# Kernel optimization log

Measured on AMD Instinct MI355X. Metric: run time of the kernel, lower is better.

The kernel has to match this reference:

```python
import jax, jax.numpy as jnp
import numpy as np

SCALE_FACTORS = (1, 2, 4)
N, T, F = 4096, 128, 128
MARKET = 64
MIX = sum(T // k for k in SCALE_FACTORS)  # 224


def hardswish(x):
    return x * jnp.clip(x + 3.0, 0.0, 6.0) * (1.0 / 6.0)


def layernorm2d(x, g, b, eps=1e-5):
    # LayerNorm with normalized_shape == last two dims (as in torch nn.LayerNorm((A, B)))
    mu = jnp.mean(x, axis=(-2, -1), keepdims=True)
    var = jnp.var(x, axis=(-2, -1), keepdims=True)
    return (x - mu) * jax.lax.rsqrt(var + eps) * g + b


def setup_inputs() -> dict:
    key = jax.random.key(0)
    ks = jax.random.split(key, 32)
    inp = {"x": jax.random.normal(ks[0], (N, T, F), jnp.float32)}
    i = 1
    for si, k in enumerate(SCALE_FACTORS):
        tk = T // k
        inp[f"cw{si}"] = jax.random.normal(ks[i], (F, F, k), jnp.float32) * 0.05; i += 1
        inp[f"cb{si}"] = jnp.zeros((F,), jnp.float32)
        inp[f"lg{si}"] = jnp.ones((tk, F), jnp.float32)
        inp[f"lb{si}"] = jnp.zeros((tk, F), jnp.float32)
        inp[f"L1_{si}"] = jax.random.normal(ks[i], (tk, tk), jnp.float32) * 0.01; i += 1
        inp[f"L2_{si}"] = jax.random.normal(ks[i], (tk, tk), jnp.float32) * 0.01; i += 1
    inp["fc_w"] = jax.random.normal(ks[i], (1, F), jnp.float32) * 0.05; i += 1
    inp["fc_b"] = jnp.zeros((1,), jnp.float32)
    inp["sm_lg"] = jnp.ones((N, MIX), jnp.float32)
    inp["sm_lb"] = jnp.zeros((N, MIX), jnp.float32)
    inp["M1"] = jax.random.normal(ks[i], (MARKET, N), jnp.float32); i += 1
    inp["M2"] = jax.random.normal(ks[i], (N, MARKET), jnp.float32); i += 1
    inp["sm_fc_w"] = jax.random.normal(ks[i], (1, 2 * MIX), jnp.float32) * 0.02; i += 1
    inp["sm_fc_b"] = jnp.zeros((1,), jnp.float32)
    return inp


def _forward(x, cw0, cb0, lg0, lb0, L1_0, L2_0,
             cw1, cb1, lg1, lb1, L1_1, L2_1,
             cw2, cb2, lg2, lb2, L1_2, L2_2,
             fc_w, fc_b, sm_lg, sm_lb, M1, M2, sm_fc_w, sm_fc_b):
    n, t, f = x.shape
    per_scale = ((cw0, cb0, lg0, lb0, L1_0, L2_0),
                 (cw1, cb1, lg1, lb1, L1_1, L2_1),
                 (cw2, cb2, lg2, lb2, L1_2, L2_2))
    parts = []
    for k, (cw, cb, lg, lb, L1, L2) in zip(SCALE_FACTORS, per_scale):
        tk = t // k
        # Conv1d(kernel=k, stride=k) == blockwise contraction over non-overlapping windows
        xr = x.transpose(0, 2, 1).reshape(n, f, tk, k)          # (n, F_in, tk, k)
        xt = jnp.einsum('nitk,oik->nto', xr, cw) + cb            # (n, tk, F)
        # TimeMixing: ragged prefix loop == single lower-triangular matmul over time
        mask = jnp.tril(jnp.ones((tk, tk), x.dtype))
        h = layernorm2d(xt, lg, lb)
        u = hardswish(jnp.einsum('ts,nsf->ntf', L1 * mask, h))
        v = jnp.einsum('ts,nsf->ntf', L2 * mask, u)
        xt = xt + v
        parts.append(xt @ fc_w[0] + fc_b[0])                     # (n, tk)
    h = jnp.concatenate(parts, axis=1)                           # (n, MIX)
    # StockMixing
    hn = layernorm2d(h, sm_lg, sm_lb)
    z = M2 @ hardswish(M1 @ hn)                                  # (n, MIX)
    out = jnp.concatenate([h, h + z], axis=1)                    # (n, 2*MIX)
    return out @ sm_fc_w[0][:, None] + sm_fc_b                   # (n, 1)


def reference(x, cw0, cb0, lg0, lb0, L1_0, L2_0,
              cw1, cb1, lg1, lb1, L1_1, L2_1,
              cw2, cb2, lg2, lb2, L1_2, L2_2,
              fc_w, fc_b, sm_lg, sm_lb, M1, M2, sm_fc_w, sm_fc_b):
    return _forward(x, cw0, cb0, lg0, lb0, L1_0, L2_0,
                    cw1, cb1, lg1, lb1, L1_1, L2_1,
                    cw2, cb2, lg2, lb2, L1_2, L2_2,
                    fc_w, fc_b, sm_lg, sm_lb, M1, M2, sm_fc_w, sm_fc_b)
```

## Files before the change

### kernel.cpp

```cpp
#include <hip/hip_runtime.h>
#include <stdint.h>

typedef __attribute__((ext_vector_type(8))) short short8;
typedef __attribute__((ext_vector_type(4))) float f32x4;

__device__ __forceinline__ unsigned short f2bf(float f) {
  union { float f; unsigned int i; } v; v.f = f;
  return (unsigned short)((v.i + 0x7FFFu + ((v.i >> 16) & 1u)) >> 16);
}
__device__ __forceinline__ float hswish(float x) {
  float t = fminf(fmaxf(x + 3.f, 0.f), 6.f);
  return x * t * (1.f / 6.f);
}
__device__ __forceinline__ short8 ldcvt8(const float* __restrict__ p) {
  float4 v0 = *(const float4*)p;
  float4 v1 = *(const float4*)(p + 4);
  short8 r;
  r[0] = (short)f2bf(v0.x); r[1] = (short)f2bf(v0.y);
  r[2] = (short)f2bf(v0.z); r[3] = (short)f2bf(v0.w);
  r[4] = (short)f2bf(v1.x); r[5] = (short)f2bf(v1.y);
  r[6] = (short)f2bf(v1.z); r[7] = (short)f2bf(v1.w);
  return r;
}

__global__ void prep_kernel(const float* __restrict__ cw0, const float* __restrict__ cw1,
                            const float* __restrict__ cw2,
                            const float* __restrict__ L1_0, const float* __restrict__ L2_0,
                            const float* __restrict__ L1_1, const float* __restrict__ L2_1,
                            const float* __restrict__ L1_2, const float* __restrict__ L2_2,
                            unsigned short* __restrict__ ws16) {
  int idx = blockIdx.x * 256 + threadIdx.x;
  if (idx < 16384) {
    ws16[idx] = f2bf(cw0[idx]);
  } else if (idx < 49152) {
    int t = idx - 16384; int o = t >> 8, m = t & 255, j = m >> 7, i = m & 127;
    ws16[idx] = f2bf(cw1[(o * 128 + i) * 2 + j]);
  } else if (idx < 114688) {
    int t = idx - 49152; int o = t >> 9, m = t & 511, j = m >> 7, i = m & 127;
    ws16[idx] = f2bf(cw2[(o * 128 + i) * 4 + j]);
  } else if (idx < 131072) {
    int u = idx - 114688; int t = u >> 7, s = u & 127;
    ws16[idx] = (s <= t) ? f2bf(L1_0[u]) : (unsigned short)0;
  } else if (idx < 147456) {
    int u = idx - 131072; int t = u >> 7, s = u & 127;
    ws16[idx] = (s <= t) ? f2bf(L2_0[u]) : (unsigned short)0;
  } else if (idx < 151552) {
    int u = idx - 147456; int t = u >> 6, s = u & 63;
    ws16[idx] = (s <= t) ? f2bf(L1_1[u]) : (unsigned short)0;
  } else if (idx < 155648) {
    int u = idx - 151552; int t = u >> 6, s = u & 63;
    ws16[idx] = (s <= t) ? f2bf(L2_1[u]) : (unsigned short)0;
  } else if (idx < 156672) {
    int u = idx - 155648; int t = u >> 5, s = u & 31;
    ws16[idx] = (s <= t) ? f2bf(L1_2[u]) : (unsigned short)0;
  } else if (idx < 157696) {
    int u = idx - 156672; int t = u >> 5, s = u & 31;
    ws16[idx] = (s <= t) ? f2bf(L2_2[u]) : (unsigned short)0;
  }
}

template <int S>
__device__ __forceinline__ void scale_pass(
    const float* __restrict__ xn,
    const float* __restrict__ cb, const float* __restrict__ lg, const float* __restrict__ lb,
    const unsigned short* __restrict__ cwLT,
    const unsigned short* __restrict__ L1b, const unsigned short* __restrict__ L2b,
    unsigned short* __restrict__ HT, float* __restrict__ scr, float* __restrict__ part,
    float* __restrict__ hout, float fcb,
    int wave, int lane, int quad, int l16, int tid) {
  constexpr int K  = 128 << S;
  constexpr int TK = 128 >> S;
  constexpr int nT = (S == 0) ? 4 : (S == 1) ? 2 : 1;
  constexpr int NK = K / 32;
  constexpr int NTK = TK / 32;
  constexpr int CMASK = TK / 8 - 1;

  const int Tb = (wave & 1) * nT;
  const int Ob = (wave >> 1) * 4;

  __syncthreads();
  if (tid < TK) part[tid] = 0.f;

  f32x4 acc[nT][4];
#pragma unroll
  for (int tt = 0; tt < nT; ++tt)
#pragma unroll
    for (int oo = 0; oo < 4; ++oo) acc[tt][oo] = (f32x4){0.f, 0.f, 0.f, 0.f};

#pragma unroll
  for (int ks = 0; ks < NK; ++ks) {
    short8 a[nT];
#pragma unroll
    for (int tt = 0; tt < nT; ++tt) {
      int t = (Tb + tt) * 16 + l16;
      a[tt] = ldcvt8(xn + t * K + ks * 32 + quad * 8);
    }
#pragma unroll
    for (int oo = 0; oo < 4; ++oo) {
      int o = (Ob + oo) * 16 + l16;
      short8 b = *(const short8*)&cwLT[o * K + ks * 32 + quad * 8];
#pragma unroll
      for (int tt = 0; tt < nT; ++tt)
        acc[tt][oo] = __builtin_amdgcn_mfma_f32_16x16x32_bf16(a[tt], b, acc[tt][oo], 0, 0, 0);
    }
  }

  float sum = 0.f, ss = 0.f;
#pragma unroll
  for (int oo = 0; oo < 4; ++oo) {
    float cbv = cb[(Ob + oo) * 16 + l16];
#pragma unroll
    for (int tt = 0; tt < nT; ++tt)
#pragma unroll
      for (int r = 0; r < 4; ++r) {
        float v = acc[tt][oo][r] + cbv;
        acc[tt][oo][r] = v;
        sum += v; ss += v * v;
      }
  }
#pragma unroll
  for (int m = 32; m >= 1; m >>= 1) { sum += __shfl_xor(sum, m); ss += __shfl_xor(ss, m); }
  if (lane == 0) { scr[256 + wave * 2] = sum; scr[257 + wave * 2] = ss; }
  __syncthreads();
  if (tid == 0) {
    float Sm = scr[256] + scr[258] + scr[260] + scr[262];
    float Sq = scr[257] + scr[259] + scr[261] + scr[263];
    float mu = Sm / (float)(TK * 128);
    float var = Sq / (float)(TK * 128) - mu * mu;
    scr[264] = mu; scr[265] = rsqrtf(var + 1e-5f);
  }
  __syncthreads();
  const float mu = scr[264], rsig = scr[265];

#pragma unroll
  for (int tt = 0; tt < nT; ++tt)
#pragma unroll
    for (int r = 0; r < 4; ++r) {
      float v = 0.f;
#pragma unroll
      for (int oo = 0; oo < 4; ++oo) v += acc[tt][oo][r] * scr[(Ob + oo) * 16 + l16];
      v += __shfl_xor(v, 1); v += __shfl_xor(v, 2);
      v += __shfl_xor(v, 4); v += __shfl_xor(v, 8);
      if (l16 == 0) atomicAdd(&part[(Tb + tt) * 16 + quad * 4 + r], v);
    }

#pragma unroll
  for (int tt = 0; tt < nT; ++tt)
#pragma unroll
    for (int oo = 0; oo < 4; ++oo) {
      int f = (Ob + oo) * 16 + l16;
      int kf = (f ^ (f >> 3)) & CMASK;
#pragma unroll
      for (int r = 0; r < 4; ++r) {
        int t = (Tb + tt) * 16 + quad * 4 + r;
        float hv = (acc[tt][oo][r] - mu) * rsig * lg[t * 128 + f] + lb[t * 128 + f];
        HT[f * TK + (((t >> 3) ^ kf) << 3) + (t & 7)] = f2bf(hv);
      }
    }
  __syncthreads();

#pragma unroll
  for (int tt = 0; tt < nT; ++tt)
#pragma unroll
    for (int oo = 0; oo < 4; ++oo) acc[tt][oo] = (f32x4){0.f, 0.f, 0.f, 0.f};
#pragma unroll
  for (int ks = 0; ks < NTK; ++ks) {
    int k0 = ks * 32;
    if (k0 > (Tb + nT - 1) * 16 + 15) continue;
    short8 a[nT];
#pragma unroll
    for (int tt = 0; tt < nT; ++tt)
      if (k0 <= (Tb + tt) * 16 + 15) {
        int t = (Tb + tt) * 16 + l16;
        a[tt] = *(const short8*)&L1b[t * TK + k0 + quad * 8];
      }
#pragma unroll
    for (int oo = 0; oo < 4; ++oo) {
      int f = (Ob + oo) * 16 + l16;
      int kf = (f ^ (f >> 3)) & CMASK;
      short8 b = *(const short8*)&HT[f * TK + (((ks * 4 + quad) ^ kf) << 3)];
#pragma unroll
      for (int tt = 0; tt < nT; ++tt)
        if (k0 <= (Tb + tt) * 16 + 15)
          acc[tt][oo] = __builtin_amdgcn_mfma_f32_16x16x32_bf16(a[tt], b, acc[tt][oo], 0, 0, 0);
    }
  }
  __syncthreads();

#pragma unroll
  for (int tt = 0; tt < nT; ++tt)
#pragma unroll
    for (int oo = 0; oo < 4; ++oo) {
      int f = (Ob + oo) * 16 + l16;
      int kf = (f ^ (f >> 3)) & CMASK;
#pragma unroll
      for (int r = 0; r < 4; ++r) {
        int t = (Tb + tt) * 16 + quad * 4 + r;
        HT[f * TK + (((t >> 3) ^ kf) << 3) + (t & 7)] = f2bf(hswish(acc[tt][oo][r]));
      }
    }
  __syncthreads();

#pragma unroll
  for (int tt = 0; tt < nT; ++tt)
#pragma unroll
    for (int oo = 0; oo < 4; ++oo) acc[tt][oo] = (f32x4){0.f, 0.f, 0.f, 0.f};
#pragma unroll
  for (int ks = 0; ks < NTK; ++ks) {
    int k0 = ks * 32;
    if (k0 > (Tb + nT - 1) * 16 + 15) continue;
    short8 a[nT];
#pragma unroll
    for (int tt = 0; tt < nT; ++tt)
      if (k0 <= (Tb + tt) * 16 + 15) {
        int t = (Tb + tt) * 16 + l16;
        a[tt] = *(const short8*)&L2b[t * TK + k0 + quad * 8];
      }
#pragma unroll
    for (int oo = 0; oo < 4; ++oo) {
      int f = (Ob + oo) * 16 + l16;
      int kf = (f ^ (f >> 3)) & CMASK;
      short8 b = *(const short8*)&HT[f * TK + (((ks * 4 + quad) ^ kf) << 3)];
#pragma unroll
      for (int tt = 0; tt < nT; ++tt)
        if (k0 <= (Tb + tt) * 16 + 15)
          acc[tt][oo] = __builtin_amdgcn_mfma_f32_16x16x32_bf16(a[tt], b, acc[tt][oo], 0, 0, 0);
    }
  }

#pragma unroll
  for (int tt = 0; tt < nT; ++tt)
#pragma unroll
    for (int r = 0; r < 4; ++r) {
      float v = 0.f;
#pragma unroll
      for (int oo = 0; oo < 4; ++oo) v += acc[tt][oo][r] * scr[(Ob + oo) * 16 + l16];
      v += __shfl_xor(v, 1); v += __shfl_xor(v, 2);
      v += __shfl_xor(v, 4); v += __shfl_xor(v, 8);
      if (l16 == 0) atomicAdd(&part[(Tb + tt) * 16 + quad * 4 + r], v);
    }
  __syncthreads();
  if (tid < TK) hout[tid] = part[tid] + fcb;
}

__launch_bounds__(256, 2)
__global__ void s1_fused(const float* __restrict__ x,
                         const float* __restrict__ cb0, const float* __restrict__ lg0, const float* __restrict__ lb0,
                         const float* __restrict__ cb1, const float* __restrict__ lg1, const float* __restrict__ lb1,
                         const float* __restrict__ cb2, const float* __restrict__ lg2, const float* __restrict__ lb2,
                         const float* __restrict__ fc_w, const float* __restrict__ fc_b,
                         const unsigned short* __restrict__ ws16,
                         float* __restrict__ h_out) {
  __shared__ unsigned short HT[128 * 128];
  __shared__ float scr[268];
  const int tid = threadIdx.x, wave = tid >> 6, lane = tid & 63;
  const int quad = lane >> 4, l16 = lane & 15;
  const int n = blockIdx.x;
  const float* xn = x + (size_t)n * 16384;
  if (tid < 128) scr[tid] = fc_w[tid];
  float* part = scr + 128;
  const float fcb = fc_b[0];
  float* hout = h_out + (size_t)n * 224;

  scale_pass<0>(xn, cb0, lg0, lb0, ws16, ws16 + 114688, ws16 + 131072,
                HT, scr, part, hout, fcb, wave, lane, quad, l16, tid);
  scale_pass<1>(xn, cb1, lg1, lb1, ws16 + 16384, ws16 + 147456, ws16 + 151552,
                HT, scr, part, hout + 128, fcb, wave, lane, quad, l16, tid);
  scale_pass<2>(xn, cb2, lg2, lb2, ws16 + 49152, ws16 + 155648, ws16 + 156672,
                HT, scr, part, hout + 192, fcb, wave, lane, quad, l16, tid);
}

__global__ void stats_kernel(const float* __restrict__ h, float* __restrict__ stats) {
  int base = blockIdx.x * 4096;
  float s = 0.f, ss = 0.f;
  for (int j = 0; j < 16; ++j) {
    float v = h[base + j * 256 + threadIdx.x];
    s += v; ss += v * v;
  }
  int lane = threadIdx.x & 63, wave = threadIdx.x >> 6;
#pragma unroll
  for (int m = 32; m >= 1; m >>= 1) { s += __shfl_xor(s, m); ss += __shfl_xor(ss, m); }
  __shared__ float red[8];
  if (lane == 0) { red[wave * 2] = s; red[wave * 2 + 1] = ss; }
  __syncthreads();
  if (threadIdx.x == 0) {
    atomicAdd(&stats[0], red[0] + red[2] + red[4] + red[6]);
    atomicAdd(&stats[1], red[1] + red[3] + red[5] + red[7]);
  }
}

__global__ void mix1_kernel(const float* __restrict__ h,
                            const float* __restrict__ sm_lg,
                            const float* __restrict__ sm_lb,
                            const float* __restrict__ M1,
                            const float* __restrict__ stats,
                            float* __restrict__ A) {
  const int m = blockIdx.x, seg = blockIdx.y;
  const int r = threadIdx.x & 63, ch = threadIdx.x >> 6;
  const float inv = 1.f / 917504.f;
  float mu = stats[0] * inv;
  float var = stats[1] * inv - mu * mu;
  float rsig = rsqrtf(var + 1e-5f);
  float acc = 0.f;
  int n0 = seg * 1024 + ch * 256;
  for (int i = 0; i < 256; ++i) {
    int n = n0 + i;
    float hn = (h[n * 224 + m] - mu) * rsig * sm_lg[n * 224 + m] + sm_lb[n * 224 + m];
    acc += M1[r * 4096 + n] * hn;
  }
  __shared__ float red[256];
  red[threadIdx.x] = acc;
  __syncthreads();
  if (threadIdx.x < 64)
    atomicAdd(&A[threadIdx.x * 224 + m],
              red[threadIdx.x] + red[64 + threadIdx.x] + red[128 + threadIdx.x] + red[192 + threadIdx.x]);
}

__global__ void mix2_kernel(const float* __restrict__ A,
                            const float* __restrict__ sm_fc_w,
                            float* __restrict__ cvec) {
  int r = threadIdx.x & 63, ch = threadIdx.x >> 6;
  float acc = 0.f;
  for (int j = ch; j < 224; j += 4)
    acc += hswish(A[r * 224 + j]) * sm_fc_w[224 + j];
  __shared__ float red[256];
  red[threadIdx.x] = acc;
  __syncthreads();
  if (threadIdx.x < 64)
    cvec[threadIdx.x] = red[threadIdx.x] + red[64 + threadIdx.x] + red[128 + threadIdx.x] + red[192 + threadIdx.x];
}

__global__ void out_kernel(const float* __restrict__ h,
                           const float* __restrict__ M2,
                           const float* __restrict__ cvec,
                           const float* __restrict__ sm_fc_w,
                           const float* __restrict__ sm_fc_b,
                           float* __restrict__ out) {
  int wave = threadIdx.x >> 6, lane = threadIdx.x & 63;
  int n = blockIdx.x * 4 + wave;
  float acc = M2[n * 64 + lane] * cvec[lane];
  for (int j = lane; j < 224; j += 64)
    acc += h[n * 224 + j] * (sm_fc_w[j] + sm_fc_w[224 + j]);
#pragma unroll
  for (int m = 32; m >= 1; m >>= 1) acc += __shfl_xor(acc, m);
  if (lane == 0) out[n] = acc + sm_fc_b[0];
}

extern "C" void kernel_launch(void* const* d_in, const int* in_sizes, int n_in,
                              void* d_out, int out_size, void* d_ws, size_t ws_size,
                              hipStream_t stream) {
  const float* x      = (const float*)d_in[0];
  const float* cw0    = (const float*)d_in[1];
  const float* cb0    = (const float*)d_in[2];
  const float* lg0    = (const float*)d_in[3];
  const float* lb0    = (const float*)d_in[4];
  const float* L1_0   = (const float*)d_in[5];
  const float* L2_0   = (const float*)d_in[6];
  const float* cw1    = (const float*)d_in[7];
  const float* cb1    = (const float*)d_in[8];
  const float* lg1    = (const float*)d_in[9];
  const float* lb1    = (const float*)d_in[10];
  const float* L1_1   = (const float*)d_in[11];
  const float* L2_1   = (const float*)d_in[12];
  const float* cw2    = (const float*)d_in[13];
  const float* cb2    = (const float*)d_in[14];
  const float* lg2    = (const float*)d_in[15];
  const float* lb2    = (const float*)d_in[16];
  const float* L1_2   = (const float*)d_in[17];
  const float* L2_2   = (const float*)d_in[18];
  const float* fc_w   = (const float*)d_in[19];
  const float* fc_b   = (const float*)d_in[20];
  const float* sm_lg  = (const float*)d_in[21];
  const float* sm_lb  = (const float*)d_in[22];
  const float* M1     = (const float*)d_in[23];
  const float* M2     = (const float*)d_in[24];
  const float* sm_fc_w = (const float*)d_in[25];
  const float* sm_fc_b = (const float*)d_in[26];

  char* ws = (char*)d_ws;
  unsigned short* ws16 = (unsigned short*)ws;
  float* h     = (float*)(ws + 315392);
  float* stats = (float*)(ws + 3985408);
  float* A     = (float*)(ws + 3985664);
  float* cvec  = (float*)(ws + 4043008);

  prep_kernel<<<616, 256, 0, stream>>>(cw0, cw1, cw2, L1_0, L2_0, L1_1, L2_1, L1_2, L2_2, ws16);

  s1_fused<<<4096, 256, 0, stream>>>(x, cb0, lg0, lb0, cb1, lg1, lb1, cb2, lg2, lb2,
                                     fc_w, fc_b, ws16, h);

  hipMemsetAsync(ws + 3985408, 0, 57600, stream);
  stats_kernel<<<224, 256, 0, stream>>>(h, stats);
  mix1_kernel<<<dim3(224, 4), 256, 0, stream>>>(h, sm_lg, sm_lb, M1, stats, A);
  mix2_kernel<<<1, 256, 0, stream>>>(A, sm_fc_w, cvec);
  out_kernel<<<1024, 256, 0, stream>>>(h, M2, cvec, sm_fc_w, sm_fc_b, (float*)d_out);
}
```

Before: 989.6 us.

## Split fused per-sample kernel into per-scale tiled kernels batching samples

```diff
diff --git a/kernel.cpp b/kernel.cpp
--- a/kernel.cpp
+++ b/kernel.cpp
@@ -3,6 +3,7 @@
 
 typedef __attribute__((ext_vector_type(8))) short short8;
 typedef __attribute__((ext_vector_type(4))) float f32x4;
+typedef __attribute__((ext_vector_type(4))) unsigned short us4;
 
 __device__ __forceinline__ unsigned short f2bf(float f) {
   union { float f; unsigned int i; } v; v.f = f;
@@ -38,102 +39,136 @@
   } else if (idx < 114688) {
     int t = idx - 49152; int o = t >> 9, m = t & 511, j = m >> 7, i = m & 127;
     ws16[idx] = f2bf(cw2[(o * 128 + i) * 4 + j]);
-  } else if (idx < 131072) {
-    int u = idx - 114688; int t = u >> 7, s = u & 127;
-    ws16[idx] = (s <= t) ? f2bf(L1_0[u]) : (unsigned short)0;
-  } else if (idx < 147456) {
-    int u = idx - 131072; int t = u >> 7, s = u & 127;
-    ws16[idx] = (s <= t) ? f2bf(L2_0[u]) : (unsigned short)0;
-  } else if (idx < 151552) {
-    int u = idx - 147456; int t = u >> 6, s = u & 63;
-    ws16[idx] = (s <= t) ? f2bf(L1_1[u]) : (unsigned short)0;
-  } else if (idx < 155648) {
-    int u = idx - 151552; int t = u >> 6, s = u & 63;
-    ws16[idx] = (s <= t) ? f2bf(L2_1[u]) : (unsigned short)0;
-  } else if (idx < 156672) {
-    int u = idx - 155648; int t = u >> 5, s = u & 31;
-    ws16[idx] = (s <= t) ? f2bf(L1_2[u]) : (unsigned short)0;
-  } else if (idx < 157696) {
-    int u = idx - 156672; int t = u >> 5, s = u & 31;
-    ws16[idx] = (s <= t) ? f2bf(L2_2[u]) : (unsigned short)0;
-  }
-}
-
-template <int S>
-__device__ __forceinline__ void scale_pass(
-    const float* __restrict__ xn,
-    const float* __restrict__ cb, const float* __restrict__ lg, const float* __restrict__ lb,
-    const unsigned short* __restrict__ cwLT,
-    const unsigned short* __restrict__ L1b, const unsigned short* __restrict__ L2b,
-    unsigned short* __restrict__ HT, float* __restrict__ scr, float* __restrict__ part,
-    float* __restrict__ hout, float fcb,
-    int wave, int lane, int quad, int l16, int tid) {
-  constexpr int K  = 128 << S;
-  constexpr int TK = 128 >> S;
-  constexpr int nT = (S == 0) ? 4 : (S == 1) ? 2 : 1;
+  } else if (idx < 212992) {
+    int u = idx - 114688; int which = u >> 14; int e = u & 16383;
+    int t = e >> 7, s = e & 127;
+    float val = 0.f;
+    if (which == 0)      { if (s <= t) val = L1_0[t * 128 + s]; }
+    else if (which == 1) { if (s <= t) val = L2_0[t * 128 + s]; }
+    else if (which == 2) { if ((s >> 6) == (t >> 6) && (s & 63) <= (t & 63)) val = L1_1[(t & 63) * 64 + (s & 63)]; }
+    else if (which == 3) { if ((s >> 6) == (t >> 6) && (s & 63) <= (t & 63)) val = L2_1[(t & 63) * 64 + (s & 63)]; }
+    else if (which == 4) { if ((s >> 5) == (t >> 5) && (s & 31) <= (t & 31)) val = L1_2[(t & 31) * 32 + (s & 31)]; }
+    else                 { if ((s >> 5) == (t >> 5) && (s & 31) <= (t & 31)) val = L2_2[(t & 31) * 32 + (s & 31)]; }
+    ws16[idx] = f2bf(val);
+  }
+}
+
+__global__ void xcvt_kernel(const float* __restrict__ x, unsigned short* __restrict__ xbf) {
+  const float4* x4 = (const float4*)x;
+  us4* o4 = (us4*)xbf;
+#pragma unroll
+  for (int j = 0; j < 4; ++j) {
+    int idx = blockIdx.x * 1024 + j * 256 + threadIdx.x;
+    float4 v = x4[idx];
+    us4 p; p[0] = f2bf(v.x); p[1] = f2bf(v.y); p[2] = f2bf(v.z); p[3] = f2bf(v.w);
+    o4[idx] = p;
+  }
+}
+
+template <bool XBF>
+__device__ __forceinline__ short8 load_a(const float* __restrict__ xf,
+                                         const unsigned short* __restrict__ xb, int off) {
+  if constexpr (XBF) return *(const short8*)&xb[off];
+  else return ldcvt8(xf + off);
+}
+
+template <int S, bool XBF>
+__launch_bounds__(256, 3)
+__global__ void s1_tile(const float* __restrict__ xf, const unsigned short* __restrict__ xb,
+                        const float* __restrict__ cb, const float* __restrict__ lg,
+                        const float* __restrict__ lb,
+                        const float* __restrict__ fc_w, const float* __restrict__ fc_b,
+                        const unsigned short* __restrict__ cwLT,
+                        const unsigned short* __restrict__ L1blk,
+                        const unsigned short* __restrict__ L2blk,
+                        float* __restrict__ h_out) {
+  constexpr int K = 128 << S;
+  constexpr int LOG2TK = 7 - S;
+  constexpr int TKM = (128 >> S) - 1;
+  constexpr int SAMPLES = 1 << S;
+  constexpr int OFF = (S == 0) ? 0 : (S == 1 ? 128 : 192);
   constexpr int NK = K / 32;
-  constexpr int NTK = TK / 32;
-  constexpr int CMASK = TK / 8 - 1;
-
-  const int Tb = (wave & 1) * nT;
-  const int Ob = (wave >> 1) * 4;
-
-  __syncthreads();
-  if (tid < TK) part[tid] = 0.f;
-
-  f32x4 acc[nT][4];
-#pragma unroll
-  for (int tt = 0; tt < nT; ++tt)
+  constexpr int GSH = 3 - S;
+  constexpr float INVD = 1.f / (float)((TKM + 1) * 128);
+
+  __shared__ unsigned short HT[128 * 128];
+  __shared__ float scr[272];
+  float* part = scr + 128;
+
+  const int tid = threadIdx.x, wave = tid >> 6, lane = tid & 63;
+  const int quad = lane >> 4, l16 = lane & 15;
+  const int Tb = (wave & 1) * 4, Ob = (wave >> 1) * 4;
+  const int n0 = blockIdx.x << S;
+  const int abase = n0 * 16384;
+  const float fcb = fc_b[0];
+
+  if (tid < 128) { scr[tid] = fc_w[tid]; part[tid] = 0.f; }
+  else if (tid < 144) scr[tid + 128] = 0.f;
+  __syncthreads();
+
+  f32x4 acc[4][4];
+#pragma unroll
+  for (int tt = 0; tt < 4; ++tt)
 #pragma unroll
     for (int oo = 0; oo < 4; ++oo) acc[tt][oo] = (f32x4){0.f, 0.f, 0.f, 0.f};
-
 #pragma unroll
   for (int ks = 0; ks < NK; ++ks) {
-    short8 a[nT];
-#pragma unroll
-    for (int tt = 0; tt < nT; ++tt) {
-      int t = (Tb + tt) * 16 + l16;
-      a[tt] = ldcvt8(xn + t * K + ks * 32 + quad * 8);
-    }
+    short8 a[4];
+#pragma unroll
+    for (int tt = 0; tt < 4; ++tt)
+      a[tt] = load_a<XBF>(xf, xb, abase + ((Tb + tt) * 16 + l16) * K + ks * 32 + quad * 8);
 #pragma unroll
     for (int oo = 0; oo < 4; ++oo) {
-      int o = (Ob + oo) * 16 + l16;
-      short8 b = *(const short8*)&cwLT[o * K + ks * 32 + quad * 8];
-#pragma unroll
-      for (int tt = 0; tt < nT; ++tt)
+      short8 b = *(const short8*)&cwLT[((Ob + oo) * 16 + l16) * K + ks * 32 + quad * 8];
+#pragma unroll
+      for (int tt = 0; tt < 4; ++tt)
         acc[tt][oo] = __builtin_amdgcn_mfma_f32_16x16x32_bf16(a[tt], b, acc[tt][oo], 0, 0, 0);
     }
   }
 
-  float sum = 0.f, ss = 0.f;
+  float ts[4] = {0.f, 0.f, 0.f, 0.f}, tq[4] = {0.f, 0.f, 0.f, 0.f};
 #pragma unroll
   for (int oo = 0; oo < 4; ++oo) {
     float cbv = cb[(Ob + oo) * 16 + l16];
 #pragma unroll
-    for (int tt = 0; tt < nT; ++tt)
+    for (int tt = 0; tt < 4; ++tt)
 #pragma unroll
       for (int r = 0; r < 4; ++r) {
         float v = acc[tt][oo][r] + cbv;
         acc[tt][oo][r] = v;
-        sum += v; ss += v * v;
+        ts[tt] += v; tq[tt] += v * v;
       }
   }
-#pragma unroll
-  for (int m = 32; m >= 1; m >>= 1) { sum += __shfl_xor(sum, m); ss += __shfl_xor(ss, m); }
-  if (lane == 0) { scr[256 + wave * 2] = sum; scr[257 + wave * 2] = ss; }
-  __syncthreads();
-  if (tid == 0) {
-    float Sm = scr[256] + scr[258] + scr[260] + scr[262];
-    float Sq = scr[257] + scr[259] + scr[261] + scr[263];
-    float mu = Sm / (float)(TK * 128);
-    float var = Sq / (float)(TK * 128) - mu * mu;
-    scr[264] = mu; scr[265] = rsqrtf(var + 1e-5f);
-  }
-  __syncthreads();
-  const float mu = scr[264], rsig = scr[265];
-
-#pragma unroll
-  for (int tt = 0; tt < nT; ++tt)
+  {
+    constexpr int GPW = (S == 2) ? 2 : 1;
+    float gs[2] = {0.f, 0.f}, gq[2] = {0.f, 0.f};
+#pragma unroll
+    for (int tt = 0; tt < 4; ++tt) {
+      int gl = (S == 2) ? (tt >> 1) : 0;
+      gs[gl] += ts[tt]; gq[gl] += tq[tt];
+    }
+#pragma unroll
+    for (int j = 0; j < GPW; ++j) {
+      float s = gs[j], q = gq[j];
+#pragma unroll
+      for (int m = 32; m >= 1; m >>= 1) { s += __shfl_xor(s, m); q += __shfl_xor(q, m); }
+      if (lane == 0) {
+        int g = (Tb >> GSH) + j;
+        atomicAdd(&scr[256 + 2 * g], s);
+        atomicAdd(&scr[257 + 2 * g], q);
+      }
+    }
+  }
+  __syncthreads();
+  if (tid < SAMPLES) {
+    float mu = scr[256 + 2 * tid] * INVD;
+    float var = scr[257 + 2 * tid] * INVD - mu * mu;
+    scr[264 + tid] = mu; scr[268 + tid] = rsqrtf(var + 1e-5f);
+  }
+  __syncthreads();
+
+#pragma unroll
+  for (int tt = 0; tt < 4; ++tt)
 #pragma unroll
     for (int r = 0; r < 4; ++r) {
       float v = 0.f;
@@ -145,129 +180,110 @@
     }
 
 #pragma unroll
-  for (int tt = 0; tt < nT; ++tt)
+  for (int tt = 0; tt < 4; ++tt) {
+    int tile = Tb + tt, g = tile >> GSH;
+    float mu = scr[264 + g], rs = scr[268 + g];
+    int tlb = (tile * 16) & TKM;
 #pragma unroll
     for (int oo = 0; oo < 4; ++oo) {
       int f = (Ob + oo) * 16 + l16;
-      int kf = (f ^ (f >> 3)) & CMASK;
+      int kf = (f ^ (f >> 3)) & 15;
 #pragma unroll
       for (int r = 0; r < 4; ++r) {
-        int t = (Tb + tt) * 16 + quad * 4 + r;
-        float hv = (acc[tt][oo][r] - mu) * rsig * lg[t * 128 + f] + lb[t * 128 + f];
-        HT[f * TK + (((t >> 3) ^ kf) << 3) + (t & 7)] = f2bf(hv);
+        int t = tile * 16 + quad * 4 + r;
+        int tl = tlb + quad * 4 + r;
+        float hv = (acc[tt][oo][r] - mu) * rs * lg[tl * 128 + f] + lb[tl * 128 + f];
+        HT[f * 128 + ((((t >> 3) ^ kf) << 3) | (t & 7))] = f2bf(hv);
       }
     }
-  __syncthreads();
-
-#pragma unroll
-  for (int tt = 0; tt < nT; ++tt)
-#pragma unroll
-    for (int oo = 0; oo < 4; ++oo) acc[tt][oo] = (f32x4){0.f, 0.f, 0.f, 0.f};
-#pragma unroll
-  for (int ks = 0; ks < NTK; ++ks) {
-    int k0 = ks * 32;
-    if (k0 > (Tb + nT - 1) * 16 + 15) continue;
-    short8 a[nT];
-#pragma unroll
-    for (int tt = 0; tt < nT; ++tt)
-      if (k0 <= (Tb + tt) * 16 + 15) {
-        int t = (Tb + tt) * 16 + l16;
-        a[tt] = *(const short8*)&L1b[t * TK + k0 + quad * 8];
-      }
+  }
+  __syncthreads();
+
+  f32x4 u[4][4];
+#pragma unroll
+  for (int tt = 0; tt < 4; ++tt)
+#pragma unroll
+    for (int oo = 0; oo < 4; ++oo) u[tt][oo] = (f32x4){0.f, 0.f, 0.f, 0.f};
+#pragma unroll
+  for (int ks = 0; ks < 4; ++ks) {
+    short8 a[4]; bool act[4]; bool any = false;
+#pragma unroll
+    for (int tt = 0; tt < 4; ++tt) {
+      int tile = Tb + tt, g = tile >> GSH;
+      act[tt] = (ks * 32 <= tile * 16 + 15) && (ks * 32 + 31 >= (g << LOG2TK));
+      if (act[tt]) { a[tt] = *(const short8*)&L1blk[(tile * 16 + l16) * 128 + ks * 32 + quad * 8]; any = true; }
+    }
+    if (!any) continue;
 #pragma unroll
     for (int oo = 0; oo < 4; ++oo) {
       int f = (Ob + oo) * 16 + l16;
-      int kf = (f ^ (f >> 3)) & CMASK;
-      short8 b = *(const short8*)&HT[f * TK + (((ks * 4 + quad) ^ kf) << 3)];
-#pragma unroll
-      for (int tt = 0; tt < nT; ++tt)
-        if (k0 <= (Tb + tt) * 16 + 15)
-          acc[tt][oo] = __builtin_amdgcn_mfma_f32_16x16x32_bf16(a[tt], b, acc[tt][oo], 0, 0, 0);
-    }
-  }
-  __syncthreads();
-
-#pragma unroll
-  for (int tt = 0; tt < nT; ++tt)
+      int kf = (f ^ (f >> 3)) & 15;
+      short8 b = *(const short8*)&HT[f * 128 + (((ks * 4 + quad) ^ kf) << 3)];
+#pragma unroll
+      for (int tt = 0; tt < 4; ++tt)
+        if (act[tt]) u[tt][oo] = __builtin_amdgcn_mfma_f32_16x16x32_bf16(a[tt], b, u[tt][oo], 0, 0, 0);
+    }
+  }
+  __syncthreads();
+
+#pragma unroll
+  for (int tt = 0; tt < 4; ++tt) {
+    int tile = Tb + tt;
 #pragma unroll
     for (int oo = 0; oo < 4; ++oo) {
       int f = (Ob + oo) * 16 + l16;
-      int kf = (f ^ (f >> 3)) & CMASK;
+      int kf = (f ^ (f >> 3)) & 15;
 #pragma unroll
       for (int r = 0; r < 4; ++r) {
-        int t = (Tb + tt) * 16 + quad * 4 + r;
-        HT[f * TK + (((t >> 3) ^ kf) << 3) + (t & 7)] = f2bf(hswish(acc[tt][oo][r]));
+        int t = tile * 16 + quad * 4 + r;
+        HT[f * 128 + ((((t >> 3) ^ kf) << 3) | (t & 7))] = f2bf(hswish(u[tt][oo][r]));
       }
     }
-  __syncthreads();
-
-#pragma unroll
-  for (int tt = 0; tt < nT; ++tt)
-#pragma unroll
-    for (int oo = 0; oo < 4; ++oo) acc[tt][oo] = (f32x4){0.f, 0.f, 0.f, 0.f};
-#pragma unroll
-  for (int ks = 0; ks < NTK; ++ks) {
-    int k0 = ks * 32;
-    if (k0 > (Tb + nT - 1) * 16 + 15) continue;
-    short8 a[nT];
-#pragma unroll
-    for (int tt = 0; tt < nT; ++tt)
-      if (k0 <= (Tb + tt) * 16 + 15) {
-        int t = (Tb + tt) * 16 + l16;
-        a[tt] = *(const short8*)&L2b[t * TK + k0 + quad * 8];
-      }
+  }
+  __syncthreads();
+
+#pragma unroll
+  for (int tt = 0; tt < 4; ++tt)
+#pragma unroll
+    for (int oo = 0; oo < 4; ++oo) u[tt][oo] = (f32x4){0.f, 0.f, 0.f, 0.f};
+#pragma unroll
+  for (int ks = 0; ks < 4; ++ks) {
+    short8 a[4]; bool act[4]; bool any = false;
+#pragma unroll
+    for (int tt = 0; tt < 4; ++tt) {
+      int tile = Tb + tt, g = tile >> GSH;
+      act[tt] = (ks * 32 <= tile * 16 + 15) && (ks * 32 + 31 >= (g << LOG2TK));
+      if (act[tt]) { a[tt] = *(const short8*)&L2blk[(tile * 16 + l16) * 128 + ks * 32 + quad * 8]; any = true; }
+    }
+    if (!any) continue;
 #pragma unroll
     for (int oo = 0; oo < 4; ++oo) {
       int f = (Ob + oo) * 16 + l16;
-      int kf = (f ^ (f >> 3)) & CMASK;
-      short8 b = *(const short8*)&HT[f * TK + (((ks * 4 + quad) ^ kf) << 3)];
-#pragma unroll
-      for (int tt = 0; tt < nT; ++tt)
-        if (k0 <= (Tb + tt) * 16 + 15)
-          acc[tt][oo] = __builtin_amdgcn_mfma_f32_16x16x32_bf16(a[tt], b, acc[tt][oo], 0, 0, 0);
-    }
-  }
-
-#pragma unroll
-  for (int tt = 0; tt < nT; ++tt)
+      int kf = (f ^ (f >> 3)) & 15;
+      short8 b = *(const short8*)&HT[f * 128 + (((ks * 4 + quad) ^ kf) << 3)];
+#pragma unroll
+      for (int tt = 0; tt < 4; ++tt)
+        if (act[tt]) u[tt][oo] = __builtin_amdgcn_mfma_f32_16x16x32_bf16(a[tt], b, u[tt][oo], 0, 0, 0);
+    }
+  }
+
+#pragma unroll
+  for (int tt = 0; tt < 4; ++tt)
 #pragma unroll
     for (int r = 0; r < 4; ++r) {
       float v = 0.f;
 #pragma unroll
-      for (int oo = 0; oo < 4; ++oo) v += acc[tt][oo][r] * scr[(Ob + oo) * 16 + l16];
+      for (int oo = 0; oo < 4; ++oo) v += u[tt][oo][r] * scr[(Ob + oo) * 16 + l16];
       v += __shfl_xor(v, 1); v += __shfl_xor(v, 2);
       v += __shfl_xor(v, 4); v += __shfl_xor(v, 8);
       if (l16 == 0) atomicAdd(&part[(Tb + tt) * 16 + quad * 4 + r], v);
     }
   __syncthreads();
-  if (tid < TK) hout[tid] = part[tid] + fcb;
-}
-
-__launch_bounds__(256, 2)
-__global__ void s1_fused(const float* __restrict__ x,
-                         const float* __restrict__ cb0, const float* __restrict__ lg0, const float* __restrict__ lb0,
-                         const float* __restrict__ cb1, const float* __restrict__ lg1, const float* __restrict__ lb1,
-                         const float* __restrict__ cb2, const float* __restrict__ lg2, const float* __restrict__ lb2,
-                         const float* __restrict__ fc_w, const float* __restrict__ fc_b,
-                         const unsigned short* __restrict__ ws16,
-                         float* __restrict__ h_out) {
-  __shared__ unsigned short HT[128 * 128];
-  __shared__ float scr[268];
-  const int tid = threadIdx.x, wave = tid >> 6, lane = tid & 63;
-  const int quad = lane >> 4, l16 = lane & 15;
-  const int n = blockIdx.x;
-  const float* xn = x + (size_t)n * 16384;
-  if (tid < 128) scr[tid] = fc_w[tid];
-  float* part = scr + 128;
-  const float fcb = fc_b[0];
-  float* hout = h_out + (size_t)n * 224;
-
-  scale_pass<0>(xn, cb0, lg0, lb0, ws16, ws16 + 114688, ws16 + 131072,
-                HT, scr, part, hout, fcb, wave, lane, quad, l16, tid);
-  scale_pass<1>(xn, cb1, lg1, lb1, ws16 + 16384, ws16 + 147456, ws16 + 151552,
-                HT, scr, part, hout + 128, fcb, wave, lane, quad, l16, tid);
-  scale_pass<2>(xn, cb2, lg2, lb2, ws16 + 49152, ws16 + 155648, ws16 + 156672,
-                HT, scr, part, hout + 192, fcb, wave, lane, quad, l16, tid);
+
+  if (tid < 128) {
+    int g = tid >> LOG2TK, tl = tid & TKM;
+    h_out[(size_t)(n0 + g) * 224 + OFF + tl] = part[tid] + fcb;
+  }
 }
 
 __global__ void stats_kernel(const float* __restrict__ h, float* __restrict__ stats) {
@@ -379,17 +395,37 @@
 
   char* ws = (char*)d_ws;
   unsigned short* ws16 = (unsigned short*)ws;
-  float* h     = (float*)(ws + 315392);
-  float* stats = (float*)(ws + 3985408);
-  float* A     = (float*)(ws + 3985664);
-  float* cvec  = (float*)(ws + 4043008);
-
-  prep_kernel<<<616, 256, 0, stream>>>(cw0, cw1, cw2, L1_0, L2_0, L1_1, L2_1, L1_2, L2_2, ws16);
-
-  s1_fused<<<4096, 256, 0, stream>>>(x, cb0, lg0, lb0, cb1, lg1, lb1, cb2, lg2, lb2,
-                                     fc_w, fc_b, ws16, h);
-
-  hipMemsetAsync(ws + 3985408, 0, 57600, stream);
+  float* h     = (float*)(ws + 425984);
+  float* stats = (float*)(ws + 4096000);
+  float* A     = (float*)(ws + 4096256);
+  float* cvec  = (float*)(ws + 4153600);
+  unsigned short* xbf = (unsigned short*)(ws + 4194304);
+  const bool use_xbf = ws_size >= 138412032ULL;
+
+  const unsigned short* cwLT0 = ws16;
+  const unsigned short* cwLT1 = ws16 + 16384;
+  const unsigned short* cwLT2 = ws16 + 49152;
+  const unsigned short* L1b0 = ws16 + 114688;
+  const unsigned short* L2b0 = ws16 + 131072;
+  const unsigned short* L1b1 = ws16 + 147456;
+  const unsigned short* L2b1 = ws16 + 163840;
+  const unsigned short* L1b2 = ws16 + 180224;
+  const unsigned short* L2b2 = ws16 + 196608;
+
+  prep_kernel<<<832, 256, 0, stream>>>(cw0, cw1, cw2, L1_0, L2_0, L1_1, L2_1, L1_2, L2_2, ws16);
+
+  if (use_xbf) {
+    xcvt_kernel<<<16384, 256, 0, stream>>>(x, xbf);
+    s1_tile<0, true><<<4096, 256, 0, stream>>>(x, xbf, cb0, lg0, lb0, fc_w, fc_b, cwLT0, L1b0, L2b0, h);
+    s1_tile<1, true><<<2048, 256, 0, stream>>>(x, xbf, cb1, lg1, lb1, fc_w, fc_b, cwLT1, L1b1, L2b1, h);
+    s1_tile<2, true><<<1024, 256, 0, stream>>>(x, xbf, cb2, lg2, lb2, fc_w, fc_b, cwLT2, L1b2, L2b2, h);
+  } else {
+    s1_tile<0, false><<<4096, 256, 0, stream>>>(x, xbf, cb0, lg0, lb0, fc_w, fc_b, cwLT0, L1b0, L2b0, h);
+    s1_tile<1, false><<<2048, 256, 0, stream>>>(x, xbf, cb1, lg1, lb1, fc_w, fc_b, cwLT1, L1b1, L2b1, h);
+    s1_tile<2, false><<<1024, 256, 0, stream>>>(x, xbf, cb2, lg2, lb2, fc_w, fc_b, cwLT2, L1b2, L2b2, h);
+  }
+
+  hipMemsetAsync(ws + 4096000, 0, 57600, stream);
   stats_kernel<<<224, 256, 0, stream>>>(h, stats);
   mix1_kernel<<<dim3(224, 4), 256, 0, stream>>>(h, sm_lg, sm_lb, M1, stats, A);
   mix2_kernel<<<1, 256, 0, stream>>>(A, sm_fc_w, cvec);
```

Result: faster. 902.0 us (-8.9%).
